# Kernel tuning notes

Measured on AMD Instinct MI355X. Metric: run time of the kernel, lower is better.

## Reference

```python
import jax, jax.numpy as jnp
import numpy as np

B, N, D = 4, 2048, 256
H = 8
HD = D // H
FF = 1024
EPS = 1e-5


def layer_norm(x, g, b):
    mu = jnp.mean(x, axis=-1, keepdims=True)
    var = jnp.mean((x - mu) ** 2, axis=-1, keepdims=True)
    return (x - mu) * jax.lax.rsqrt(var + EPS) * g + b


def setup_inputs() -> dict:
    key = jax.random.key(0)
    ks = jax.random.split(key, 12)
    s = 0.02
    return {
        "tokens": jax.random.normal(ks[0], (B, N, D), dtype=jnp.float32),
        "key_padding_mask": jnp.zeros((B, N), dtype=bool),
        "ln1_g": jnp.ones((D,), jnp.float32),
        "ln1_b": jnp.zeros((D,), jnp.float32),
        "wq": jax.random.normal(ks[1], (D, D), jnp.float32) * s,
        "bq": jnp.zeros((D,), jnp.float32),
        "wk": jax.random.normal(ks[2], (D, D), jnp.float32) * s,
        "bk": jnp.zeros((D,), jnp.float32),
        "wv": jax.random.normal(ks[3], (D, D), jnp.float32) * s,
        "bv": jnp.zeros((D,), jnp.float32),
        "wo": jax.random.normal(ks[4], (D, D), jnp.float32) * s,
        "bo": jnp.zeros((D,), jnp.float32),
        "ln2_g": jnp.ones((D,), jnp.float32),
        "ln2_b": jnp.zeros((D,), jnp.float32),
        "w1": jax.random.normal(ks[5], (D, FF), jnp.float32) * s,
        "b1": jnp.zeros((FF,), jnp.float32),
        "w2": jax.random.normal(ks[6], (FF, D), jnp.float32) * s,
        "b2": jnp.zeros((D,), jnp.float32),
    }


def reference(tokens, key_padding_mask, ln1_g, ln1_b, wq, bq, wk, bk, wv, bv,
              wo, bo, ln2_g, ln2_b, w1, b1, w2, b2):
    x = tokens
    # --- self-attention sublayer (pre-LN) ---
    xn = layer_norm(x, ln1_g, ln1_b)
    q = (xn @ wq + bq).reshape(B, N, H, HD).transpose(0, 2, 1, 3)  # [B,H,N,HD]
    k = (xn @ wk + bk).reshape(B, N, H, HD).transpose(0, 2, 1, 3)
    v = (xn @ wv + bv).reshape(B, N, H, HD).transpose(0, 2, 1, 3)
    scores = jnp.einsum('bhqd,bhkd->bhqk', q, k) / np.sqrt(HD).astype(np.float32)
    scores = jnp.where(key_padding_mask[:, None, None, :], -jnp.inf, scores)
    probs = jax.nn.softmax(scores, axis=-1)
    attn = jnp.einsum('bhqk,bhkd->bhqd', probs, v)
    attn = attn.transpose(0, 2, 1, 3).reshape(B, N, D)
    x = x + (attn @ wo + bo)
    # --- feed-forward sublayer (pre-LN) ---
    xn2 = layer_norm(x, ln2_g, ln2_b)
    h = jax.nn.gelu(xn2 @ w1 + b1, approximate=False)  # torch GELU is exact erf
    x = x + (h @ w2 + b2)
    return x
```

## Files before the change

### kernel.cpp

```cpp
#include <hip/hip_runtime.h>
#include <cmath>

typedef __attribute__((ext_vector_type(8))) __bf16 bf16x8;
typedef __attribute__((ext_vector_type(4))) __bf16 bf16x4;
typedef __attribute__((ext_vector_type(4))) float  f32x4;

constexpr int NB   = 4;
constexpr int SEQ  = 2048;
constexpr int DM   = 256;
constexpr int NH   = 8;
constexpr int DH   = 32;
constexpr int DFF  = 1024;
constexpr int MTOK = NB * SEQ;

__global__ __launch_bounds__(256) void ln_kernel(const float* __restrict__ x,
                                                 const float* __restrict__ g,
                                                 const float* __restrict__ b,
                                                 __bf16* __restrict__ out) {
  int wave = threadIdx.x >> 6, lane = threadIdx.x & 63;
  int row = blockIdx.x * 4 + wave;
  const float* xr = x + (size_t)row * DM;
  f32x4 v = *(const f32x4*)(xr + lane * 4);
  float s  = v[0] + v[1] + v[2] + v[3];
  float sq = v[0]*v[0] + v[1]*v[1] + v[2]*v[2] + v[3]*v[3];
  #pragma unroll
  for (int off = 1; off < 64; off <<= 1) {
    s  += __shfl_xor(s, off);
    sq += __shfl_xor(sq, off);
  }
  float mu  = s * (1.0f / DM);
  float var = sq * (1.0f / DM) - mu * mu;
  float rs  = rsqrtf(var + 1e-5f);
  f32x4 gv = *(const f32x4*)(g + lane * 4);
  f32x4 bv = *(const f32x4*)(b + lane * 4);
  bf16x4 o;
  #pragma unroll
  for (int i = 0; i < 4; ++i) o[i] = (__bf16)((v[i] - mu) * rs * gv[i] + bv[i]);
  *(bf16x4*)(out + (size_t)row * DM + lane * 4) = o;
}

__global__ __launch_bounds__(256) void prep_kernel(
    const float* __restrict__ wq, const float* __restrict__ wk, const float* __restrict__ wv,
    const float* __restrict__ wo, const float* __restrict__ w1, const float* __restrict__ w2,
    const unsigned char* __restrict__ mask, const float* __restrict__ tokens,
    const float* __restrict__ ln1g, const float* __restrict__ ln1b,
    __bf16* __restrict__ wqkvT, __bf16* __restrict__ woT,
    __bf16* __restrict__ w1T, __bf16* __restrict__ w2T,
    float* __restrict__ madd_g, __bf16* __restrict__ xn1) {
  __shared__ float tile[32][33];
  int bid = blockIdx.x;
  int tid = threadIdx.x;
  if (bid >= 800) {
    int row = (bid - 800) * 4 + (tid >> 6);
    int lane = tid & 63;
    const float* xr = tokens + (size_t)row * DM;
    f32x4 v = *(const f32x4*)(xr + lane * 4);
    float s  = v[0] + v[1] + v[2] + v[3];
    float sq = v[0]*v[0] + v[1]*v[1] + v[2]*v[2] + v[3]*v[3];
    #pragma unroll
    for (int off = 1; off < 64; off <<= 1) {
      s  += __shfl_xor(s, off);
      sq += __shfl_xor(sq, off);
    }
    float mu  = s * (1.0f / DM);
    float var = sq * (1.0f / DM) - mu * mu;
    float rs  = rsqrtf(var + 1e-5f);
    f32x4 gv = *(const f32x4*)(ln1g + lane * 4);
    f32x4 bv = *(const f32x4*)(ln1b + lane * 4);
    bf16x4 o;
    #pragma unroll
    for (int i = 0; i < 4; ++i) o[i] = (__bf16)((v[i] - mu) * rs * gv[i] + bv[i]);
    *(bf16x4*)(xn1 + (size_t)row * DM + lane * 4) = o;
    return;
  }
  if (bid >= 768) {
    int idx = (bid - 768) * 256 + tid;
    madd_g[idx] = mask[idx] ? -__builtin_inff() : 0.0f;
    return;
  }
  const float* W; __bf16* Wt; int K, N, n0, k0;
  if (bid < 256) {
    int z = bid >> 6, local = bid & 63;
    K = 256; N = 256;
    n0 = (local & 7) * 32; k0 = (local >> 3) * 32;
    if      (z == 0) { W = wq; Wt = wqkvT;          }
    else if (z == 1) { W = wk; Wt = wqkvT + 65536;  }
    else if (z == 2) { W = wv; Wt = wqkvT + 131072; }
    else             { W = wo; Wt = woT;            }
  } else if (bid < 512) {
    int local = bid - 256;
    W = w1; Wt = w1T; K = 256; N = 1024;
    n0 = (local & 31) * 32; k0 = (local >> 5) * 32;
  } else {
    int local = bid - 512;
    W = w2; Wt = w2T; K = 1024; N = 256;
    n0 = (local & 7) * 32; k0 = (local >> 3) * 32;
  }
  {
    int kl = tid >> 3, n4 = (tid & 7) * 4;
    f32x4 v = *(const f32x4*)(W + (size_t)(k0 + kl) * N + n0 + n4);
    tile[kl][n4 + 0] = v[0]; tile[kl][n4 + 1] = v[1];
    tile[kl][n4 + 2] = v[2]; tile[kl][n4 + 3] = v[3];
  }
  __syncthreads();
  {
    int nl = tid >> 3, k4 = (tid & 7) * 4;
    bf16x4 o;
    #pragma unroll
    for (int i = 0; i < 4; ++i) o[i] = (__bf16)tile[k4 + i][nl];
    *(bf16x4*)(Wt + (size_t)(n0 + nl) * K + k0 + k4) = o;
  }
}

template<int BM, int BN, int EP, int AF = 0>
__global__ __launch_bounds__(256) void gemm_bt(
    const __bf16* __restrict__ A, const __bf16* __restrict__ Bt,
    int M, int N, int K,
    const float* __restrict__ bias,
    const float* __restrict__ bq, const float* __restrict__ bk, const float* __restrict__ bv,
    const float* __restrict__ resid, float* __restrict__ outf,
    __bf16* __restrict__ outb,
    __bf16* __restrict__ outq, __bf16* __restrict__ outk, __bf16* __restrict__ outv,
    const float* __restrict__ Af = nullptr, const float* __restrict__ lpart = nullptr) {
  constexpr int MT = BM / 32, NT = BN / 32;
  constexpr int AP = BM / 32, BP = BN / 32;
  __shared__ __bf16 As[BM * 64];
  __shared__ __bf16 Bs[BN * 64];
  int tid = threadIdx.x;
  int wave = tid >> 6, lane = tid & 63;
  int wm = wave >> 1, wn = wave & 1;
  int quad = lane >> 4, l16 = lane & 15;
  int m0 = blockIdx.x * BM, n0 = blockIdx.y * BN;
  int lrow = lane >> 3;
  int lcg  = ((lane & 7) ^ lrow) * 8;

  auto loadA = [&](int rbase, int kcol) -> bf16x8 {
    int gr = m0 + rbase + lrow;
    if constexpr (AF == 0) {
      return *(const bf16x8*)(A + (size_t)gr * K + kcol);
    } else {
      const float* p0 = Af + (size_t)gr * K + kcol;
      const float* p1 = p0 + (size_t)MTOK * DM;
      f32x4 a0 = *(const f32x4*)p0, a0b = *(const f32x4*)(p0 + 4);
      f32x4 a1 = *(const f32x4*)p1, a1b = *(const f32x4*)(p1 + 4);
      int bb = gr >> 11, tok = gr & 2047, hh = kcol >> 5;
      float l = lpart[((size_t)bb * NH + hh) * SEQ + tok] +
                lpart[(((size_t)NB + bb) * NH + hh) * SEQ + tok];
      float inv = 1.0f / l;
      bf16x8 o;
      #pragma unroll
      for (int i = 0; i < 4; ++i) {
        o[i]     = (__bf16)((a0[i]  + a1[i])  * inv);
        o[i + 4] = (__bf16)((a0b[i] + a1b[i]) * inv);
      }
      return o;
    }
  };

  f32x4 acc[MT][NT];
  #pragma unroll
  for (int mt = 0; mt < MT; ++mt)
    #pragma unroll
    for (int nt = 0; nt < NT; ++nt)
      #pragma unroll
      for (int r = 0; r < 4; ++r) acc[mt][nt][r] = 0.0f;

  bf16x8 ap[AP], bp[BP];
  #pragma unroll
  for (int i = 0; i < AP; ++i) ap[i] = loadA(wave * (BM / 4) + i * 8, lcg);
  #pragma unroll
  for (int i = 0; i < BP; ++i) {
    int rbase = wave * (BN / 4) + i * 8;
    bp[i] = *(const bf16x8*)(Bt + (size_t)(n0 + rbase + lrow) * K + lcg);
  }
  #pragma unroll
  for (int i = 0; i < AP; ++i) {
    int rbase = wave * (BM / 4) + i * 8;
    *(bf16x8*)&As[rbase * 64 + lane * 8] = ap[i];
  }
  #pragma unroll
  for (int i = 0; i < BP; ++i) {
    int rbase = wave * (BN / 4) + i * 8;
    *(bf16x8*)&Bs[rbase * 64 + lane * 8] = bp[i];
  }
  __syncthreads();

  for (int kt = 0; kt < K; kt += 64) {
    bool more = (kt + 64) < K;
    if (more) {
      #pragma unroll
      for (int i = 0; i < AP; ++i) ap[i] = loadA(wave * (BM / 4) + i * 8, kt + 64 + lcg);
      #pragma unroll
      for (int i = 0; i < BP; ++i) {
        int rbase = wave * (BN / 4) + i * 8;
        bp[i] = *(const bf16x8*)(Bt + (size_t)(n0 + rbase + lrow) * K + kt + 64 + lcg);
      }
    }
    #pragma unroll
    for (int ks = 0; ks < 2; ++ks) {
      bf16x8 af[MT], bfr[NT];
      #pragma unroll
      for (int mt = 0; mt < MT; ++mt) {
        int row = wm * (BM / 2) + mt * 16 + l16;
        af[mt] = *(const bf16x8*)&As[row * 64 + (((ks * 4 + quad) ^ (l16 & 7)) * 8)];
      }
      #pragma unroll
      for (int nt = 0; nt < NT; ++nt) {
        int row = wn * (BN / 2) + nt * 16 + l16;
        bfr[nt] = *(const bf16x8*)&Bs[row * 64 + (((ks * 4 + quad) ^ (l16 & 7)) * 8)];
      }
      #pragma unroll
      for (int mt = 0; mt < MT; ++mt)
        #pragma unroll
        for (int nt = 0; nt < NT; ++nt)
          acc[mt][nt] = __builtin_amdgcn_mfma_f32_16x16x32_bf16(af[mt], bfr[nt], acc[mt][nt], 0, 0, 0);
    }
    if (more) {
      __syncthreads();
      #pragma unroll
      for (int i = 0; i < AP; ++i) {
        int rbase = wave * (BM / 4) + i * 8;
        *(bf16x8*)&As[rbase * 64 + lane * 8] = ap[i];
      }
      #pragma unroll
      for (int i = 0; i < BP; ++i) {
        int rbase = wave * (BN / 4) + i * 8;
        *(bf16x8*)&Bs[rbase * 64 + lane * 8] = bp[i];
      }
      __syncthreads();
    }
  }

  #pragma unroll
  for (int mt = 0; mt < MT; ++mt)
  #pragma unroll
  for (int nt = 0; nt < NT; ++nt)
  #pragma unroll
  for (int r = 0; r < 4; ++r) {
    int gm = m0 + wm * (BM / 2) + mt * 16 + quad * 4 + r;
    int gn = n0 + wn * (BN / 2) + nt * 16 + l16;
    float v = acc[mt][nt][r];
    if constexpr (EP == 0) {
      int which = gn >> 8, nn = gn & 255;
      const float* bp2 = which == 0 ? bq : (which == 1 ? bk : bv);
      v += bp2[nn];
      int h = nn >> 5, hd = nn & 31;
      int bb = gm >> 11, tok = gm & 2047;
      if (which == 2) {
        outv[(((size_t)(bb * NH + h)) * DH + hd) * SEQ + tok] = (__bf16)v;
      } else {
        __bf16* dst = which == 0 ? outq : outk;
        dst[(((size_t)(bb * NH + h)) * SEQ + tok) * DH + hd] = (__bf16)v;
      }
    } else if constexpr (EP == 1) {
      v += bias[gn] + resid[(size_t)gm * N + gn];
      outf[(size_t)gm * N + gn] = v;
    } else {
      v += bias[gn];
      float v2 = v * v;
      float t = __builtin_amdgcn_exp2f(v * (2.3022082f + 0.10294324f * v2));
      outb[(size_t)gm * N + gn] = (__bf16)(v * t * __builtin_amdgcn_rcpf(t + 1.0f));
    }
  }
}

__global__ __launch_bounds__(256) void attn_kernel(
    const __bf16* __restrict__ Q, const __bf16* __restrict__ K,
    const __bf16* __restrict__ Vt, const float* __restrict__ madd_g,
    float* __restrict__ Opart, float* __restrict__ lpart) {
  constexpr float C2 = 0.2550350030061664f;
  __shared__ __bf16 Ks[128][36];
  __shared__ __bf16 Vs[32][132];
  __shared__ __bf16 Ps[4][2][16][68];
  int bh = blockIdx.y;
  int q0 = blockIdx.x * 128;
  int half = blockIdx.z;
  int b  = bh >> 3, h = bh & 7;
  int tid = threadIdx.x;
  int wave = tid >> 6, lane = tid & 63;
  int quad = lane >> 4, l16 = lane & 15;
  const __bf16* Qb = Q  + (size_t)bh * SEQ * DH;
  const __bf16* Kb = K  + (size_t)bh * SEQ * DH;
  const __bf16* Vb = Vt + (size_t)bh * DH * SEQ;
  const float* maddb = madd_g + b * SEQ;
  int qw = q0 + wave * 32;
  int kbase = half * (SEQ / 2);

  bf16x8 qf[2];
  #pragma unroll
  for (int qg = 0; qg < 2; ++qg)
    qf[qg] = *(const bf16x8*)(Qb + (size_t)(qw + qg * 16 + l16) * DH + quad * 8);

  bf16x8 ones;
  #pragma unroll
  for (int i = 0; i < 8; ++i) ones[i] = (__bf16)1.0f;

  f32x4 o[2][2], ol[2];
  #pragma unroll
  for (int qg = 0; qg < 2; ++qg) {
    #pragma unroll
    for (int nt = 0; nt < 2; ++nt)
      #pragma unroll
      for (int r = 0; r < 4; ++r) o[qg][nt][r] = 0.0f;
    #pragma unroll
    for (int r = 0; r < 4; ++r) ol[qg][r] = 0.0f;
  }

  f32x4 zf; zf[0] = zf[1] = zf[2] = zf[3] = 0.0f;

  for (int st = 0; st < 8; ++st) {
    int kb0 = kbase + st * 128;
    __syncthreads();
    #pragma unroll
    for (int p = 0; p < 2; ++p) {
      int c = p * 256 + tid, row = c >> 2, cg = (c & 3) * 8;
      *(bf16x8*)&Ks[row][cg] = *(const bf16x8*)(Kb + (size_t)(kb0 + row) * DH + cg);
    }
    #pragma unroll
    for (int p = 0; p < 2; ++p) {
      int c = p * 256 + tid, row = c >> 4, cg = (c & 15) * 8;
      *(bf16x8*)&Vs[row][cg] = *(const bf16x8*)(Vb + (size_t)row * SEQ + kb0 + cg);
    }
    __syncthreads();

    #pragma unroll
    for (int sub = 0; sub < 2; ++sub) {
      int kl = sub * 64;
      f32x4 s[2][4];
      #pragma unroll
      for (int mt = 0; mt < 4; ++mt) {
        bf16x8 kf = *(const bf16x8*)&Ks[kl + mt * 16 + l16][quad * 8];
        s[0][mt] = __builtin_amdgcn_mfma_f32_16x16x32_bf16(kf, qf[0], zf, 0, 0, 0);
        s[1][mt] = __builtin_amdgcn_mfma_f32_16x16x32_bf16(kf, qf[1], zf, 0, 0, 0);
      }
      #pragma unroll
      for (int mt = 0; mt < 4; ++mt) {
        f32x4 md = *(const f32x4*)(maddb + kb0 + kl + mt * 16 + quad * 4);
        #pragma unroll
        for (int qg = 0; qg < 2; ++qg) {
          bf16x4 pv;
          #pragma unroll
          for (int r = 0; r < 4; ++r)
            pv[r] = (__bf16)__builtin_amdgcn_exp2f(fmaf(s[qg][mt][r], C2, md[r]));
          *(bf16x4*)&Ps[wave][qg][l16][mt * 16 + quad * 4] = pv;
        }
      }
      #pragma unroll
      for (int ks = 0; ks < 2; ++ks) {
        bf16x8 vf[2];
        #pragma unroll
        for (int nt = 0; nt < 2; ++nt)
          vf[nt] = *(const bf16x8*)&Vs[nt * 16 + l16][kl + ks * 32 + quad * 8];
        #pragma unroll
        for (int qg = 0; qg < 2; ++qg) {
          bf16x8 pf = *(const bf16x8*)&Ps[wave][qg][l16][ks * 32 + quad * 8];
          #pragma unroll
          for (int nt = 0; nt < 2; ++nt)
            o[qg][nt] = __builtin_amdgcn_mfma_f32_16x16x32_bf16(pf, vf[nt], o[qg][nt], 0, 0, 0);
          ol[qg] = __builtin_amdgcn_mfma_f32_16x16x32_bf16(pf, ones, ol[qg], 0, 0, 0);
        }
      }
    }
  }

  float* Op = Opart + (size_t)half * MTOK * DM;
  #pragma unroll
  for (int qg = 0; qg < 2; ++qg) {
    #pragma unroll
    for (int nt = 0; nt < 2; ++nt)
      #pragma unroll
      for (int r = 0; r < 4; ++r) {
        int q   = qw + qg * 16 + quad * 4 + r;
        int col = h * DH + nt * 16 + l16;
        Op[((size_t)(b * SEQ + q)) * DM + col] = o[qg][nt][r];
      }
    if (l16 == 0) {
      #pragma unroll
      for (int r = 0; r < 4; ++r)
        lpart[((((size_t)half * NB + b) * NH) + h) * SEQ + qw + qg * 16 + quad * 4 + r] = ol[qg][r];
    }
  }
}

extern "C" void kernel_launch(void* const* d_in, const int* in_sizes, int n_in,
                              void* d_out, int out_size, void* d_ws, size_t ws_size,
                              hipStream_t stream) {
  const float* tokens = (const float*)d_in[0];
  const unsigned char* mask = (const unsigned char*)d_in[1];
  const float* ln1g = (const float*)d_in[2];
  const float* ln1b = (const float*)d_in[3];
  const float* wq = (const float*)d_in[4];
  const float* bq = (const float*)d_in[5];
  const float* wk = (const float*)d_in[6];
  const float* bk = (const float*)d_in[7];
  const float* wv = (const float*)d_in[8];
  const float* bv = (const float*)d_in[9];
  const float* wo = (const float*)d_in[10];
  const float* bo = (const float*)d_in[11];
  const float* ln2g = (const float*)d_in[12];
  const float* ln2b = (const float*)d_in[13];
  const float* w1 = (const float*)d_in[14];
  const float* b1 = (const float*)d_in[15];
  const float* w2 = (const float*)d_in[16];
  const float* b2 = (const float*)d_in[17];
  float* out = (float*)d_out;
  char* ws = (char*)d_ws;

  __bf16* wqkvT = (__bf16*)(ws + 0);
  __bf16* woT   = (__bf16*)(ws + 393216);
  __bf16* w1T   = (__bf16*)(ws + 524288);
  __bf16* w2T   = (__bf16*)(ws + 1048576);
  __bf16* xn1   = (__bf16*)(ws + 1572864);
  float*  lpart = (float*)(ws + 1572864);
  __bf16* qb    = (__bf16*)(ws + 5767168);
  __bf16* kb    = (__bf16*)(ws + 9961472);
  __bf16* vt    = (__bf16*)(ws + 18350080);
  float*  x1    = (float*)(ws + 26738688);
  __bf16* xn2   = (__bf16*)(ws + 35127296);
  __bf16* hbuf  = (__bf16*)(ws + 39321600);
  float*  Opart = (float*)(ws + 39321600);
  float*  madd  = (float*)(ws + 56098816);

  prep_kernel<<<2848, 256, 0, stream>>>(
      wq, wk, wv, wo, w1, w2, mask, tokens, ln1g, ln1b,
      wqkvT, woT, w1T, w2T, madd, xn1);

  gemm_bt<128, 64, 0><<<dim3(64, 12), 256, 0, stream>>>(
      xn1, wqkvT, MTOK, 768, 256, nullptr, bq, bk, bv,
      nullptr, nullptr, nullptr, qb, kb, vt);

  attn_kernel<<<dim3(SEQ / 128, 32, 2), 256, 0, stream>>>(qb, kb, vt, madd, Opart, lpart);

  gemm_bt<64, 64, 1, 1><<<dim3(128, 4), 256, 0, stream>>>(
      nullptr, woT, MTOK, 256, 256, bo, nullptr, nullptr, nullptr,
      tokens, x1, nullptr, nullptr, nullptr, nullptr, Opart, lpart);

  ln_kernel<<<MTOK / 4, 256, 0, stream>>>(x1, ln2g, ln2b, xn2);

  gemm_bt<128, 128, 2><<<dim3(64, 8), 256, 0, stream>>>(
      xn2, w1T, MTOK, DFF, 256, b1, nullptr, nullptr, nullptr,
      nullptr, nullptr, hbuf, nullptr, nullptr, nullptr);

  gemm_bt<64, 64, 1><<<dim3(128, 4), 256, 0, stream>>>(
      hbuf, w2T, MTOK, 256, DFF, b2, nullptr, nullptr, nullptr,
      x1, out, nullptr, nullptr, nullptr, nullptr);
}
```

Measured before the change: 187.3 us.

## Merge all layer stages into one cooperative persistent kernel with grid syncs

Replaces seven separate kernel launches with a single cooperative persistent kernel that loops over virtual blocks for each stage, separated by grid-wide barriers. It also changes the FF1 GEMM tile from 128x128 to 128x64. The aim is to remove launch overhead and inter-kernel gaps between stages. The cost is a shared LDS allocation sized for the largest stage, which limits occupancy, plus the cost of the grid barriers. A fallback path launches the stages as separate kernels if the cooperative launch fails.

```diff
diff --git a/kernel.cpp b/kernel.cpp
--- a/kernel.cpp
+++ b/kernel.cpp
@@ -1,5 +1,8 @@
 #include <hip/hip_runtime.h>
+#include <hip/hip_cooperative_groups.h>
 #include <cmath>
+
+namespace cg = cooperative_groups;
 
 typedef __attribute__((ext_vector_type(8))) __bf16 bf16x8;
 typedef __attribute__((ext_vector_type(4))) __bf16 bf16x4;
@@ -13,13 +16,23 @@
 constexpr int DFF  = 1024;
 constexpr int MTOK = NB * SEQ;
 
-__global__ __launch_bounds__(256) void ln_kernel(const float* __restrict__ x,
-                                                 const float* __restrict__ g,
-                                                 const float* __restrict__ b,
-                                                 __bf16* __restrict__ out) {
-  int wave = threadIdx.x >> 6, lane = threadIdx.x & 63;
-  int row = blockIdx.x * 4 + wave;
-  const float* xr = x + (size_t)row * DM;
+struct MegaArgs {
+  const float* tokens; const unsigned char* mask;
+  const float* ln1g; const float* ln1b;
+  const float* wq; const float* bq; const float* wk; const float* bk;
+  const float* wv; const float* bv; const float* wo; const float* bo;
+  const float* ln2g; const float* ln2b;
+  const float* w1; const float* b1; const float* w2; const float* b2;
+  float* out;
+  __bf16* wqkvT; __bf16* woT; __bf16* w1T; __bf16* w2T;
+  __bf16* xn1; __bf16* qb; __bf16* kb; __bf16* vt; __bf16* xn2; __bf16* hbuf;
+  float* lpart; float* x1; float* Opart; float* madd;
+};
+
+__device__ __forceinline__ void ln_row(const float* __restrict__ xr,
+                                       const float* __restrict__ g,
+                                       const float* __restrict__ b,
+                                       __bf16* __restrict__ outr, int lane) {
   f32x4 v = *(const f32x4*)(xr + lane * 4);
   float s  = v[0] + v[1] + v[2] + v[3];
   float sq = v[0]*v[0] + v[1]*v[1] + v[2]*v[2] + v[3]*v[3];
@@ -36,64 +49,37 @@
   bf16x4 o;
   #pragma unroll
   for (int i = 0; i < 4; ++i) o[i] = (__bf16)((v[i] - mu) * rs * gv[i] + bv[i]);
-  *(bf16x4*)(out + (size_t)row * DM + lane * 4) = o;
-}
-
-__global__ __launch_bounds__(256) void prep_kernel(
-    const float* __restrict__ wq, const float* __restrict__ wk, const float* __restrict__ wv,
-    const float* __restrict__ wo, const float* __restrict__ w1, const float* __restrict__ w2,
-    const unsigned char* __restrict__ mask, const float* __restrict__ tokens,
-    const float* __restrict__ ln1g, const float* __restrict__ ln1b,
-    __bf16* __restrict__ wqkvT, __bf16* __restrict__ woT,
-    __bf16* __restrict__ w1T, __bf16* __restrict__ w2T,
-    float* __restrict__ madd_g, __bf16* __restrict__ xn1) {
-  __shared__ float tile[32][33];
-  int bid = blockIdx.x;
-  int tid = threadIdx.x;
+  *(bf16x4*)(outr + lane * 4) = o;
+}
+
+__device__ void prep_vb(int bid, int tid, char* smem, const MegaArgs& a) {
   if (bid >= 800) {
     int row = (bid - 800) * 4 + (tid >> 6);
-    int lane = tid & 63;
-    const float* xr = tokens + (size_t)row * DM;
-    f32x4 v = *(const f32x4*)(xr + lane * 4);
-    float s  = v[0] + v[1] + v[2] + v[3];
-    float sq = v[0]*v[0] + v[1]*v[1] + v[2]*v[2] + v[3]*v[3];
-    #pragma unroll
-    for (int off = 1; off < 64; off <<= 1) {
-      s  += __shfl_xor(s, off);
-      sq += __shfl_xor(sq, off);
-    }
-    float mu  = s * (1.0f / DM);
-    float var = sq * (1.0f / DM) - mu * mu;
-    float rs  = rsqrtf(var + 1e-5f);
-    f32x4 gv = *(const f32x4*)(ln1g + lane * 4);
-    f32x4 bv = *(const f32x4*)(ln1b + lane * 4);
-    bf16x4 o;
-    #pragma unroll
-    for (int i = 0; i < 4; ++i) o[i] = (__bf16)((v[i] - mu) * rs * gv[i] + bv[i]);
-    *(bf16x4*)(xn1 + (size_t)row * DM + lane * 4) = o;
+    ln_row(a.tokens + (size_t)row * DM, a.ln1g, a.ln1b, a.xn1 + (size_t)row * DM, tid & 63);
     return;
   }
   if (bid >= 768) {
     int idx = (bid - 768) * 256 + tid;
-    madd_g[idx] = mask[idx] ? -__builtin_inff() : 0.0f;
+    a.madd[idx] = a.mask[idx] ? -__builtin_inff() : 0.0f;
     return;
   }
+  float (*tile)[33] = (float(*)[33])smem;
   const float* W; __bf16* Wt; int K, N, n0, k0;
   if (bid < 256) {
     int z = bid >> 6, local = bid & 63;
     K = 256; N = 256;
     n0 = (local & 7) * 32; k0 = (local >> 3) * 32;
-    if      (z == 0) { W = wq; Wt = wqkvT;          }
-    else if (z == 1) { W = wk; Wt = wqkvT + 65536;  }
-    else if (z == 2) { W = wv; Wt = wqkvT + 131072; }
-    else             { W = wo; Wt = woT;            }
+    if      (z == 0) { W = a.wq; Wt = a.wqkvT;          }
+    else if (z == 1) { W = a.wk; Wt = a.wqkvT + 65536;  }
+    else if (z == 2) { W = a.wv; Wt = a.wqkvT + 131072; }
+    else             { W = a.wo; Wt = a.woT;            }
   } else if (bid < 512) {
     int local = bid - 256;
-    W = w1; Wt = w1T; K = 256; N = 1024;
+    W = a.w1; Wt = a.w1T; K = 256; N = 1024;
     n0 = (local & 31) * 32; k0 = (local >> 5) * 32;
   } else {
     int local = bid - 512;
-    W = w2; Wt = w2T; K = 1024; N = 256;
+    W = a.w2; Wt = a.w2T; K = 1024; N = 256;
     n0 = (local & 7) * 32; k0 = (local >> 3) * 32;
   }
   {
@@ -110,27 +96,25 @@
     for (int i = 0; i < 4; ++i) o[i] = (__bf16)tile[k4 + i][nl];
     *(bf16x4*)(Wt + (size_t)(n0 + nl) * K + k0 + k4) = o;
   }
-}
-
-template<int BM, int BN, int EP, int AF = 0>
-__global__ __launch_bounds__(256) void gemm_bt(
-    const __bf16* __restrict__ A, const __bf16* __restrict__ Bt,
-    int M, int N, int K,
+  __syncthreads();
+}
+
+template<int BM, int BN, int EP, int AF>
+__device__ void gemm_phase(int bx, int by, int tid, char* smem,
+    const __bf16* __restrict__ A, const __bf16* __restrict__ Bt, int N, int K,
     const float* __restrict__ bias,
     const float* __restrict__ bq, const float* __restrict__ bk, const float* __restrict__ bv,
-    const float* __restrict__ resid, float* __restrict__ outf,
-    __bf16* __restrict__ outb,
+    const float* __restrict__ resid, float* __restrict__ outf, __bf16* __restrict__ outb,
     __bf16* __restrict__ outq, __bf16* __restrict__ outk, __bf16* __restrict__ outv,
-    const float* __restrict__ Af = nullptr, const float* __restrict__ lpart = nullptr) {
+    const float* __restrict__ Af, const float* __restrict__ lpart) {
   constexpr int MT = BM / 32, NT = BN / 32;
   constexpr int AP = BM / 32, BP = BN / 32;
-  __shared__ __bf16 As[BM * 64];
-  __shared__ __bf16 Bs[BN * 64];
-  int tid = threadIdx.x;
+  __bf16* As = (__bf16*)smem;
+  __bf16* Bs = (__bf16*)(smem + (size_t)BM * 64 * sizeof(__bf16));
   int wave = tid >> 6, lane = tid & 63;
   int wm = wave >> 1, wn = wave & 1;
   int quad = lane >> 4, l16 = lane & 15;
-  int m0 = blockIdx.x * BM, n0 = blockIdx.y * BN;
+  int m0 = bx * BM, n0 = by * BN;
   int lrow = lane >> 3;
   int lcg  = ((lane & 7) ^ lrow) * 8;
 
@@ -262,27 +246,22 @@
       outb[(size_t)gm * N + gn] = (__bf16)(v * t * __builtin_amdgcn_rcpf(t + 1.0f));
     }
   }
-}
-
-__global__ __launch_bounds__(256) void attn_kernel(
-    const __bf16* __restrict__ Q, const __bf16* __restrict__ K,
-    const __bf16* __restrict__ Vt, const float* __restrict__ madd_g,
-    float* __restrict__ Opart, float* __restrict__ lpart) {
+  __syncthreads();
+}
+
+__device__ void attn_phase(int qc, int bh, int half, int tid, char* smem, const MegaArgs& a) {
   constexpr float C2 = 0.2550350030061664f;
-  __shared__ __bf16 Ks[128][36];
-  __shared__ __bf16 Vs[32][132];
-  __shared__ __bf16 Ps[4][2][16][68];
-  int bh = blockIdx.y;
-  int q0 = blockIdx.x * 128;
-  int half = blockIdx.z;
+  __bf16 (*Ks)[36]        = (__bf16(*)[36])smem;
+  __bf16 (*Vs)[132]       = (__bf16(*)[132])(smem + 9216);
+  __bf16 (*Ps)[2][16][68] = (__bf16(*)[2][16][68])(smem + 17664);
+  int q0 = qc * 128;
   int b  = bh >> 3, h = bh & 7;
-  int tid = threadIdx.x;
   int wave = tid >> 6, lane = tid & 63;
   int quad = lane >> 4, l16 = lane & 15;
-  const __bf16* Qb = Q  + (size_t)bh * SEQ * DH;
-  const __bf16* Kb = K  + (size_t)bh * SEQ * DH;
-  const __bf16* Vb = Vt + (size_t)bh * DH * SEQ;
-  const float* maddb = madd_g + b * SEQ;
+  const __bf16* Qb = a.qb + (size_t)bh * SEQ * DH;
+  const __bf16* Kb = a.kb + (size_t)bh * SEQ * DH;
+  const __bf16* Vb = a.vt + (size_t)bh * DH * SEQ;
+  const float* maddb = a.madd + b * SEQ;
   int qw = q0 + wave * 32;
   int kbase = half * (SEQ / 2);
 
@@ -313,13 +292,13 @@
     __syncthreads();
     #pragma unroll
     for (int p = 0; p < 2; ++p) {
-      int c = p * 256 + tid, row = c >> 2, cg = (c & 3) * 8;
-      *(bf16x8*)&Ks[row][cg] = *(const bf16x8*)(Kb + (size_t)(kb0 + row) * DH + cg);
+      int c = p * 256 + tid, row = c >> 2, cg2 = (c & 3) * 8;
+      *(bf16x8*)&Ks[row][cg2] = *(const bf16x8*)(Kb + (size_t)(kb0 + row) * DH + cg2);
     }
     #pragma unroll
     for (int p = 0; p < 2; ++p) {
-      int c = p * 256 + tid, row = c >> 4, cg = (c & 15) * 8;
-      *(bf16x8*)&Vs[row][cg] = *(const bf16x8*)(Vb + (size_t)row * SEQ + kb0 + cg);
+      int c = p * 256 + tid, row = c >> 4, cg2 = (c & 15) * 8;
+      *(bf16x8*)&Vs[row][cg2] = *(const bf16x8*)(Vb + (size_t)row * SEQ + kb0 + cg2);
     }
     __syncthreads();
 
@@ -363,7 +342,7 @@
     }
   }
 
-  float* Op = Opart + (size_t)half * MTOK * DM;
+  float* Op = a.Opart + (size_t)half * MTOK * DM;
   #pragma unroll
   for (int qg = 0; qg < 2; ++qg) {
     #pragma unroll
@@ -377,71 +356,137 @@
     if (l16 == 0) {
       #pragma unroll
       for (int r = 0; r < 4; ++r)
-        lpart[((((size_t)half * NB + b) * NH) + h) * SEQ + qw + qg * 16 + quad * 4 + r] = ol[qg][r];
-    }
-  }
+        a.lpart[((((size_t)half * NB + b) * NH) + h) * SEQ + qw + qg * 16 + quad * 4 + r] = ol[qg][r];
+    }
+  }
+  __syncthreads();
+}
+
+__device__ __forceinline__ void phase_qkv(int vb, int tid, char* smem, const MegaArgs& a) {
+  gemm_phase<128, 64, 0, 0>(vb & 63, vb >> 6, tid, smem,
+      a.xn1, a.wqkvT, 768, 256, nullptr, a.bq, a.bk, a.bv,
+      nullptr, nullptr, nullptr, a.qb, a.kb, a.vt, nullptr, nullptr);
+}
+__device__ __forceinline__ void phase_wo(int vb, int tid, char* smem, const MegaArgs& a) {
+  gemm_phase<64, 64, 1, 1>(vb & 127, vb >> 7, tid, smem,
+      nullptr, a.woT, 256, 256, a.bo, nullptr, nullptr, nullptr,
+      a.tokens, a.x1, nullptr, nullptr, nullptr, nullptr, a.Opart, a.lpart);
+}
+__device__ __forceinline__ void phase_ff1(int vb, int tid, char* smem, const MegaArgs& a) {
+  gemm_phase<128, 64, 2, 0>(vb & 63, vb >> 6, tid, smem,
+      a.xn2, a.w1T, 1024, 256, a.b1, nullptr, nullptr, nullptr,
+      nullptr, nullptr, a.hbuf, nullptr, nullptr, nullptr, nullptr, nullptr);
+}
+__device__ __forceinline__ void phase_ff2(int vb, int tid, char* smem, const MegaArgs& a) {
+  gemm_phase<64, 64, 1, 0>(vb & 127, vb >> 7, tid, smem,
+      a.hbuf, a.w2T, 256, 1024, a.b2, nullptr, nullptr, nullptr,
+      a.x1, a.out, nullptr, nullptr, nullptr, nullptr, nullptr, nullptr);
+}
+
+__global__ __launch_bounds__(256, 4) void mega_kernel(MegaArgs a) {
+  __shared__ __align__(16) char smem[35072];
+  cg::grid_group grid = cg::this_grid();
+  int rb = blockIdx.x, nb = gridDim.x;
+  int tid = threadIdx.x;
+
+  for (int vb = rb; vb < 2848; vb += nb) prep_vb(vb, tid, smem, a);
+  grid.sync();
+  for (int vb = rb; vb < 768; vb += nb) phase_qkv(vb, tid, smem, a);
+  grid.sync();
+  for (int vb = rb; vb < 1024; vb += nb)
+    attn_phase(vb & 15, (vb >> 4) & 31, vb >> 9, tid, smem, a);
+  grid.sync();
+  for (int vb = rb; vb < 512; vb += nb) phase_wo(vb, tid, smem, a);
+  grid.sync();
+  for (int vb = rb; vb < 2048; vb += nb) {
+    int row = vb * 4 + (tid >> 6);
+    ln_row(a.x1 + (size_t)row * DM, a.ln2g, a.ln2b, a.xn2 + (size_t)row * DM, tid & 63);
+  }
+  grid.sync();
+  for (int vb = rb; vb < 1024; vb += nb) phase_ff1(vb, tid, smem, a);
+  grid.sync();
+  for (int vb = rb; vb < 512; vb += nb) phase_ff2(vb, tid, smem, a);
+}
+
+__global__ __launch_bounds__(256) void prep_k(MegaArgs a) {
+  __shared__ __align__(16) char smem[4224];
+  prep_vb(blockIdx.x, threadIdx.x, smem, a);
+}
+__global__ __launch_bounds__(256) void qkv_k(MegaArgs a) {
+  __shared__ __align__(16) char smem[24576];
+  phase_qkv(blockIdx.y * 64 + blockIdx.x, threadIdx.x, smem, a);
+}
+__global__ __launch_bounds__(256) void attn_k(MegaArgs a) {
+  __shared__ __align__(16) char smem[35072];
+  attn_phase(blockIdx.x, blockIdx.y, blockIdx.z, threadIdx.x, smem, a);
+}
+__global__ __launch_bounds__(256) void wo_k(MegaArgs a) {
+  __shared__ __align__(16) char smem[16384];
+  phase_wo(blockIdx.y * 128 + blockIdx.x, threadIdx.x, smem, a);
+}
+__global__ __launch_bounds__(256) void ln2_k(MegaArgs a) {
+  int row = blockIdx.x * 4 + (threadIdx.x >> 6);
+  ln_row(a.x1 + (size_t)row * DM, a.ln2g, a.ln2b, a.xn2 + (size_t)row * DM, threadIdx.x & 63);
+}
+__global__ __launch_bounds__(256) void ff1_k(MegaArgs a) {
+  __shared__ __align__(16) char smem[24576];
+  phase_ff1(blockIdx.y * 64 + blockIdx.x, threadIdx.x, smem, a);
+}
+__global__ __launch_bounds__(256) void ff2_k(MegaArgs a) {
+  __shared__ __align__(16) char smem[16384];
+  phase_ff2(blockIdx.y * 128 + blockIdx.x, threadIdx.x, smem, a);
 }
 
 extern "C" void kernel_launch(void* const* d_in, const int* in_sizes, int n_in,
                               void* d_out, int out_size, void* d_ws, size_t ws_size,
                               hipStream_t stream) {
-  const float* tokens = (const float*)d_in[0];
-  const unsigned char* mask = (const unsigned char*)d_in[1];
-  const float* ln1g = (const float*)d_in[2];
-  const float* ln1b = (const float*)d_in[3];
-  const float* wq = (const float*)d_in[4];
-  const float* bq = (const float*)d_in[5];
-  const float* wk = (const float*)d_in[6];
-  const float* bk = (const float*)d_in[7];
-  const float* wv = (const float*)d_in[8];
-  const float* bv = (const float*)d_in[9];
-  const float* wo = (const float*)d_in[10];
-  const float* bo = (const float*)d_in[11];
-  const float* ln2g = (const float*)d_in[12];
-  const float* ln2b = (const float*)d_in[13];
-  const float* w1 = (const float*)d_in[14];
-  const float* b1 = (const float*)d_in[15];
-  const float* w2 = (const float*)d_in[16];
-  const float* b2 = (const float*)d_in[17];
-  float* out = (float*)d_out;
   char* ws = (char*)d_ws;
-
-  __bf16* wqkvT = (__bf16*)(ws + 0);
-  __bf16* woT   = (__bf16*)(ws + 393216);
-  __bf16* w1T   = (__bf16*)(ws + 524288);
-  __bf16* w2T   = (__bf16*)(ws + 1048576);
-  __bf16* xn1   = (__bf16*)(ws + 1572864);
-  float*  lpart = (float*)(ws + 1572864);
-  __bf16* qb    = (__bf16*)(ws + 5767168);
-  __bf16* kb    = (__bf16*)(ws + 9961472);
-  __bf16* vt    = (__bf16*)(ws + 18350080);
-  float*  x1    = (float*)(ws + 26738688);
-  __bf16* xn2   = (__bf16*)(ws + 35127296);
-  __bf16* hbuf  = (__bf16*)(ws + 39321600);
-  float*  Opart = (float*)(ws + 39321600);
-  float*  madd  = (float*)(ws + 56098816);
-
-  prep_kernel<<<2848, 256, 0, stream>>>(
-      wq, wk, wv, wo, w1, w2, mask, tokens, ln1g, ln1b,
-      wqkvT, woT, w1T, w2T, madd, xn1);
-
-  gemm_bt<128, 64, 0><<<dim3(64, 12), 256, 0, stream>>>(
-      xn1, wqkvT, MTOK, 768, 256, nullptr, bq, bk, bv,
-      nullptr, nullptr, nullptr, qb, kb, vt);
-
-  attn_kernel<<<dim3(SEQ / 128, 32, 2), 256, 0, stream>>>(qb, kb, vt, madd, Opart, lpart);
-
-  gemm_bt<64, 64, 1, 1><<<dim3(128, 4), 256, 0, stream>>>(
-      nullptr, woT, MTOK, 256, 256, bo, nullptr, nullptr, nullptr,
-      tokens, x1, nullptr, nullptr, nullptr, nullptr, Opart, lpart);
-
-  ln_kernel<<<MTOK / 4, 256, 0, stream>>>(x1, ln2g, ln2b, xn2);
-
-  gemm_bt<128, 128, 2><<<dim3(64, 8), 256, 0, stream>>>(
-      xn2, w1T, MTOK, DFF, 256, b1, nullptr, nullptr, nullptr,
-      nullptr, nullptr, hbuf, nullptr, nullptr, nullptr);
-
-  gemm_bt<64, 64, 1><<<dim3(128, 4), 256, 0, stream>>>(
-      hbuf, w2T, MTOK, 256, DFF, b2, nullptr, nullptr, nullptr,
-      x1, out, nullptr, nullptr, nullptr, nullptr);
-}
+  MegaArgs a;
+  a.tokens = (const float*)d_in[0];
+  a.mask   = (const unsigned char*)d_in[1];
+  a.ln1g = (const float*)d_in[2];  a.ln1b = (const float*)d_in[3];
+  a.wq = (const float*)d_in[4];    a.bq = (const float*)d_in[5];
+  a.wk = (const float*)d_in[6];    a.bk = (const float*)d_in[7];
+  a.wv = (const float*)d_in[8];    a.bv = (const float*)d_in[9];
+  a.wo = (const float*)d_in[10];   a.bo = (const float*)d_in[11];
+  a.ln2g = (const float*)d_in[12]; a.ln2b = (const float*)d_in[13];
+  a.w1 = (const float*)d_in[14];   a.b1 = (const float*)d_in[15];
+  a.w2 = (const float*)d_in[16];   a.b2 = (const float*)d_in[17];
+  a.out = (float*)d_out;
+
+  a.wqkvT = (__bf16*)(ws + 0);
+  a.woT   = (__bf16*)(ws + 393216);
+  a.w1T   = (__bf16*)(ws + 524288);
+  a.w2T   = (__bf16*)(ws + 1048576);
+  a.xn1   = (__bf16*)(ws + 1572864);
+  a.lpart = (float*)(ws + 1572864);
+  a.qb    = (__bf16*)(ws + 5767168);
+  a.kb    = (__bf16*)(ws + 9961472);
+  a.vt    = (__bf16*)(ws + 18350080);
+  a.x1    = (float*)(ws + 26738688);
+  a.xn2   = (__bf16*)(ws + 35127296);
+  a.hbuf  = (__bf16*)(ws + 39321600);
+  a.Opart = (float*)(ws + 39321600);
+  a.madd  = (float*)(ws + 56098816);
+
+  int maxB = 0;
+  hipError_t oe = hipOccupancyMaxActiveBlocksPerMultiprocessor(&maxB, mega_kernel, 256, 0);
+  int grid = 1024;
+  if (oe == hipSuccess && maxB >= 1) {
+    int g = maxB * 256;
+    if (g < grid) grid = g;
+  }
+
+  void* kargs[] = { (void*)&a };
+  hipError_t err = hipLaunchCooperativeKernel((const void*)mega_kernel, dim3(grid), dim3(256),
+                                              kargs, 0, stream);
+  if (err != hipSuccess) {
+    prep_k<<<2848, 256, 0, stream>>>(a);
+    qkv_k<<<dim3(64, 12), 256, 0, stream>>>(a);
+    attn_k<<<dim3(16, 32, 2), 256, 0, stream>>>(a);
+    wo_k<<<dim3(128, 4), 256, 0, stream>>>(a);
+    ln2_k<<<2048, 256, 0, stream>>>(a);
+    ff1_k<<<dim3(64, 16), 256, 0, stream>>>(a);
+    ff2_k<<<dim3(128, 4), 256, 0, stream>>>(a);
+  }
+}
```

Measured after the change: 644.2 us. 3.44x slower.
